# Kernel tuning notes

Measured on AMD Instinct MI355X. Metric: run time of the kernel, lower is better.

Reference implementation:

```python
import jax, jax.numpy as jnp
import numpy as np

B, I, M, A, HC, HR = 64, 10, 64, 16384, 256, 2
O = 8  # output_size = num_data_bits
EPS = 1e-8


def setup_inputs() -> dict:
    key = jax.random.key(0)
    ks = jax.random.split(key, 16)
    inputs = jax.random.normal(ks[0], (B, I), jnp.float32)
    # init_state: memory ~ N(0.5, 0.2)
    memory = 0.5 + 0.2 * jax.random.normal(ks[1], (B, M, A), jnp.float32)
    rw = jax.random.uniform(ks[2], (B, HR, A), jnp.float32)
    read_w = rw / rw.sum(-1, keepdims=True)           # normalized attention weights
    ww = jax.random.uniform(ks[3], (B, A), jnp.float32)
    write_w = ww / ww.sum(-1, keepdims=True)
    h = 0.1 * jax.random.normal(ks[4], (B, HC), jnp.float32)
    c = 0.1 * jax.random.normal(ks[5], (B, HC), jnp.float32)
    read_vecs = 0.1 * jax.random.normal(ks[6], (B, HR, M), jnp.float32)
    lstm_in = I + HR * M  # controller sees input ++ flattened read vectors
    sc = lambda n: 1.0 / np.sqrt(n)
    W_ih = sc(lstm_in) * jax.random.normal(ks[7], (4 * HC, lstm_in), jnp.float32)
    W_hh = sc(HC) * jax.random.normal(ks[8], (4 * HC, HC), jnp.float32)
    b_lstm = jnp.zeros((4 * HC,), jnp.float32)
    P = HR * (M + 6) + (3 * M + 6)  # 338
    W_int = sc(HC) * jax.random.normal(ks[9], (P, HC), jnp.float32)
    b_int = jnp.zeros((P,), jnp.float32)
    W_out = sc(HC) * jax.random.normal(ks[10], (O, HC), jnp.float32)
    b_out = jnp.zeros((O,), jnp.float32)
    return dict(inputs=inputs, memory=memory, read_w=read_w, write_w=write_w,
                h=h, c=c, read_vecs=read_vecs, W_ih=W_ih, W_hh=W_hh,
                b_lstm=b_lstm, W_int=W_int, b_int=b_int, W_out=W_out, b_out=b_out)


def _address(k, beta, g, s, gamma, w_prev, mem):
    """NTM addressing: content sim -> interpolate -> circular shift -> sharpen.
    k:[B,M] beta,g,gamma:[B,1] s:[B,3] w_prev:[B,A] mem:[B,M,A] -> [B,A]."""
    beta = jax.nn.softplus(beta)
    g = jax.nn.sigmoid(g)
    s = jax.nn.softmax(s, axis=-1)
    gamma = 1.0 + jax.nn.softplus(gamma)
    kn = k / (jnp.linalg.norm(k, axis=-1, keepdims=True) + EPS)
    mn = mem / (jnp.linalg.norm(mem, axis=1, keepdims=True) + EPS)
    sim = jnp.einsum('bm,bma->ba', kn, mn)          # cosine similarity
    wc = jax.nn.softmax(beta * sim, axis=-1)         # content weights
    wg = g * wc + (1.0 - g) * w_prev                 # interpolation gate
    ws = (s[:, 0:1] * jnp.roll(wg, -1, axis=-1)      # circular conv, shifts {-1,0,1}
          + s[:, 1:2] * wg
          + s[:, 2:3] * jnp.roll(wg, 1, axis=-1))
    wp = (ws + EPS) ** gamma                         # sharpening
    return wp / (wp.sum(-1, keepdims=True) + EPS)


def reference(inputs, memory, read_w, write_w, h, c, read_vecs,
              W_ih, W_hh, b_lstm, W_int, b_int, W_out, b_out):
    # --- LSTM controller: concat(input, read vectors) -> hidden ---
    x = jnp.concatenate([inputs, read_vecs.reshape(B, HR * M)], axis=-1)
    gates = x @ W_ih.T + h @ W_hh.T + b_lstm
    ig, fg, gg, og = jnp.split(gates, 4, axis=-1)
    c_new = jax.nn.sigmoid(fg) * c + jax.nn.sigmoid(ig) * jnp.tanh(gg)
    h_new = jax.nn.sigmoid(og) * jnp.tanh(c_new)
    # --- Interface parameter head ---
    p = h_new @ W_int.T + b_int
    off = 0
    read_params = []
    for _ in range(HR):
        blk = p[:, off:off + M + 6]; off += M + 6
        read_params.append((blk[:, :M], blk[:, M:M + 1], blk[:, M + 1:M + 2],
                            blk[:, M + 2:M + 5], blk[:, M + 5:M + 6]))
    wb = p[:, off:]
    kw, bw, gw, sw, gmw = wb[:, :M], wb[:, M:M + 1], wb[:, M + 1:M + 2], wb[:, M + 2:M + 5], wb[:, M + 5:M + 6]
    erase = jax.nn.sigmoid(wb[:, M + 6:2 * M + 6])   # [B,M]
    add = wb[:, 2 * M + 6:]                          # [B,M]
    # --- Write: address, erase/add rank-1 memory update ---
    w_wr = _address(kw, bw, gw, sw, gmw, write_w, memory)         # [B,A]
    mem_new = memory * (1.0 - erase[:, :, None] * w_wr[:, None, :]) \
              + add[:, :, None] * w_wr[:, None, :]
    # --- Read heads on updated memory ---
    rws, rvs = [], []
    for r in range(HR):
        w = _address(*read_params[r], read_w[:, r], mem_new)
        rws.append(w)
        rvs.append(jnp.einsum('bma,ba->bm', mem_new, w))
    logits = h_new @ W_out.T + b_out
    return (logits, mem_new, jnp.stack(rvs, 1), jnp.stack(rws, 1), w_wr, h_new, c_new)
```

## Files before the change

kernel.cpp:

```cpp
#include <hip/hip_runtime.h>
#include <math.h>

#define BB 64
#define ID 10
#define MD 64
#define AD 16384
#define HCD 256
#define HRD 2
#define OD 8
#define PD 338
#define EPSF 1e-8f

static constexpr size_t OFF_LOGITS = 0;
static constexpr size_t OFF_MEM = (size_t)BB * OD;
static constexpr size_t OFF_RVS = OFF_MEM + (size_t)BB * MD * AD;
static constexpr size_t OFF_RWS = OFF_RVS + (size_t)BB * HRD * MD;
static constexpr size_t OFF_WWR = OFF_RWS + (size_t)BB * HRD * AD;
static constexpr size_t OFF_H   = OFF_WWR + (size_t)BB * AD;
static constexpr size_t OFF_C   = OFF_H + (size_t)BB * HCD;

static constexpr size_t PAR = 0;
static constexpr size_t PAR_STR = 384;
static constexpr size_t EW   = PAR + (size_t)BB * PAR_STR;
static constexpr size_t ER   = EW + (size_t)BB * AD;
static constexpr size_t SUMS = ER + (size_t)2 * BB * AD;

__device__ __forceinline__ float sigmoidf_(float x) { return 1.f / (1.f + expf(-x)); }
__device__ __forceinline__ float softplusf_(float x) { return x > 20.f ? x : log1pf(expf(x)); }

__global__ __launch_bounds__(256) void k_small(
    const float* __restrict__ inputs, const float* __restrict__ read_vecs,
    const float* __restrict__ h, const float* __restrict__ c,
    const float* __restrict__ W_ih, const float* __restrict__ W_hh,
    const float* __restrict__ b_lstm, const float* __restrict__ W_int,
    const float* __restrict__ b_int, const float* __restrict__ W_out,
    const float* __restrict__ b_out, float* __restrict__ out,
    float* __restrict__ ws)
{
  const int b = blockIdx.x;
  const int t = threadIdx.x;
  __shared__ float sx[144];
  __shared__ float sh[HCD];
  __shared__ float sg[4 * HCD];
  __shared__ float shn[HCD];
  __shared__ float sp[PD];

  if (t < ID) sx[t] = inputs[(size_t)b * ID + t];
  else if (t < ID + HRD * MD) sx[t] = read_vecs[(size_t)b * HRD * MD + (t - ID)];
  if (t < HCD) sh[t] = h[(size_t)b * HCD + t];
  if (t < HRD * MD) out[OFF_RVS + (size_t)b * HRD * MD + t] = 0.f;
  if (t >= 128 && t < 136) ws[SUMS + (size_t)b * 8 + (t - 128)] = 0.f;
  __syncthreads();

  const int LIN = ID + HRD * MD;
  #pragma unroll
  for (int q = 0; q < 4; ++q) {
    int j = t + q * 256;
    const float* wr = W_ih + (size_t)j * LIN;
    float acc = b_lstm[j];
    for (int k = 0; k < LIN; ++k) acc += sx[k] * wr[k];
    const float* wh = W_hh + (size_t)j * HCD;
    for (int k = 0; k < HCD; ++k) acc += sh[k] * wh[k];
    sg[j] = acc;
  }
  __syncthreads();

  {
    float ig = sg[t], fg = sg[t + 256], gg = sg[t + 512], og = sg[t + 768];
    float cv = c[(size_t)b * HCD + t];
    float cn = sigmoidf_(fg) * cv + sigmoidf_(ig) * tanhf(gg);
    float hn = sigmoidf_(og) * tanhf(cn);
    shn[t] = hn;
    out[OFF_C + (size_t)b * HCD + t] = cn;
    out[OFF_H + (size_t)b * HCD + t] = hn;
  }
  __syncthreads();

  for (int j = t; j < PD; j += 256) {
    const float* wr = W_int + (size_t)j * HCD;
    float acc = b_int[j];
    for (int k = 0; k < HCD; ++k) acc += shn[k] * wr[k];
    sp[j] = acc;
  }
  if (t < OD) {
    const float* wr = W_out + (size_t)t * HCD;
    float acc = b_out[t];
    for (int k = 0; k < HCD; ++k) acc += shn[k] * wr[k];
    out[OFF_LOGITS + (size_t)b * OD + t] = acc;
  }
  __syncthreads();

  float* par = ws + PAR + (size_t)b * PAR_STR;
  const int wv = t >> 6, lane = t & 63;
  if (wv < 3) {
    const int base = (wv == 0) ? 140 : (wv - 1) * 70;
    const int slot = (wv == 0) ? 0 : (192 + (wv - 1) * 64);
    float kv = sp[base + lane];
    float ss = kv * kv;
    #pragma unroll
    for (int o = 32; o > 0; o >>= 1) ss += __shfl_xor(ss, o);
    par[slot + lane] = kv / (sqrtf(ss) + EPSF);
    if (lane == 0) {
      const int sb = (wv == 0) ? 320 : (326 + (wv - 1) * 6);
      float beta = softplusf_(sp[base + 64]);
      float g = sigmoidf_(sp[base + 65]);
      float s0 = sp[base + 66], s1 = sp[base + 67], s2 = sp[base + 68];
      float mx = fmaxf(s0, fmaxf(s1, s2));
      float e0 = expf(s0 - mx), e1 = expf(s1 - mx), e2 = expf(s2 - mx);
      float inv = 1.f / (e0 + e1 + e2);
      float gamma = 1.f + softplusf_(sp[base + 69]);
      par[sb + 0] = beta; par[sb + 1] = g;
      par[sb + 2] = e0 * inv; par[sb + 3] = e1 * inv; par[sb + 4] = e2 * inv;
      par[sb + 5] = gamma;
    }
  } else if (wv == 3) {
    par[64 + lane] = sigmoidf_(sp[210 + lane]);
    par[128 + lane] = sp[274 + lane];
  }
}

__global__ __launch_bounds__(256) void k_wsim(const float* __restrict__ mem,
                                              float* __restrict__ ws)
{
  const int b = blockIdx.y;
  const int tid = threadIdx.x;
  const size_t a0 = (size_t)blockIdx.x * 1024 + (size_t)tid * 4;
  const float* par = ws + PAR + (size_t)b * PAR_STR;
  __shared__ float kn[MD];
  if (tid < MD) kn[tid] = par[tid];
  __syncthreads();

  const float* mb = mem + (size_t)b * MD * AD + a0;
  float4 ssq = make_float4(0.f, 0.f, 0.f, 0.f);
  float4 dt  = make_float4(0.f, 0.f, 0.f, 0.f);
  for (int m = 0; m < MD; ++m) {
    float4 v = *(const float4*)(mb + (size_t)m * AD);
    float kv = kn[m];
    ssq.x += v.x * v.x; ssq.y += v.y * v.y; ssq.z += v.z * v.z; ssq.w += v.w * v.w;
    dt.x += kv * v.x;  dt.y += kv * v.y;  dt.z += kv * v.z;  dt.w += kv * v.w;
  }
  const float beta = par[320];
  float4 e;
  e.x = expf(beta * (dt.x / (sqrtf(ssq.x) + EPSF) - 1.f));
  e.y = expf(beta * (dt.y / (sqrtf(ssq.y) + EPSF) - 1.f));
  e.z = expf(beta * (dt.z / (sqrtf(ssq.z) + EPSF) - 1.f));
  e.w = expf(beta * (dt.w / (sqrtf(ssq.w) + EPSF) - 1.f));
  *(float4*)(ws + EW + (size_t)b * AD + a0) = e;

  float s = e.x + e.y + e.z + e.w;
  #pragma unroll
  for (int o = 32; o > 0; o >>= 1) s += __shfl_xor(s, o);
  __shared__ float red[4];
  if ((tid & 63) == 0) red[tid >> 6] = s;
  __syncthreads();
  if (tid == 0) atomicAdd(ws + SUMS + (size_t)b * 8 + 0, red[0] + red[1] + red[2] + red[3]);
}

__global__ __launch_bounds__(256) void k_wsharp(const float* __restrict__ write_w,
                                                float* __restrict__ out,
                                                float* __restrict__ ws)
{
  const int b = blockIdx.y;
  const int tid = threadIdx.x;
  const int a0 = blockIdx.x * 1024 + tid * 4;
  const float* par = ws + PAR + (size_t)b * PAR_STR;
  const float g = par[321], s0 = par[322], s1 = par[323], s2 = par[324], gamma = par[325];
  const float inv_se = 1.f / ws[SUMS + (size_t)b * 8 + 0];
  const float* e = ws + EW + (size_t)b * AD;
  const float* wprev = write_w + (size_t)b * AD;

  float wg[6];
  #pragma unroll
  for (int i = 0; i < 6; ++i) {
    int a = (a0 - 1 + i) & (AD - 1);
    wg[i] = g * e[a] * inv_se + (1.f - g) * wprev[a];
  }
  float4 wp;
  wp.x = powf(s0 * wg[2] + s1 * wg[1] + s2 * wg[0] + EPSF, gamma);
  wp.y = powf(s0 * wg[3] + s1 * wg[2] + s2 * wg[1] + EPSF, gamma);
  wp.z = powf(s0 * wg[4] + s1 * wg[3] + s2 * wg[2] + EPSF, gamma);
  wp.w = powf(s0 * wg[5] + s1 * wg[4] + s2 * wg[3] + EPSF, gamma);
  *(float4*)(out + OFF_WWR + (size_t)b * AD + a0) = wp;

  float s = wp.x + wp.y + wp.z + wp.w;
  #pragma unroll
  for (int o = 32; o > 0; o >>= 1) s += __shfl_xor(s, o);
  __shared__ float red[4];
  if ((tid & 63) == 0) red[tid >> 6] = s;
  __syncthreads();
  if (tid == 0) atomicAdd(ws + SUMS + (size_t)b * 8 + 1, red[0] + red[1] + red[2] + red[3]);
}

__global__ __launch_bounds__(256) void k_update(const float* __restrict__ mem,
                                                float* __restrict__ out,
                                                float* __restrict__ ws)
{
  const int b = blockIdx.y;
  const int tid = threadIdx.x;
  const size_t a0 = (size_t)blockIdx.x * 1024 + (size_t)tid * 4;
  const float* par = ws + PAR + (size_t)b * PAR_STR;
  __shared__ float se[MD], sa[MD], sk0[MD], sk1[MD];
  if (tid < MD) {
    se[tid] = par[64 + tid]; sa[tid] = par[128 + tid];
    sk0[tid] = par[192 + tid]; sk1[tid] = par[256 + tid];
  }
  __syncthreads();

  const float invw = 1.f / (ws[SUMS + (size_t)b * 8 + 1] + EPSF);
  float* wwr = out + OFF_WWR + (size_t)b * AD + a0;
  float4 w = *(float4*)wwr;
  w.x *= invw; w.y *= invw; w.z *= invw; w.w *= invw;
  *(float4*)wwr = w;

  const float* mb = mem + (size_t)b * MD * AD + a0;
  float* nb = out + OFF_MEM + (size_t)b * MD * AD + a0;
  float4 ssq = make_float4(0.f, 0.f, 0.f, 0.f);
  float4 d0 = make_float4(0.f, 0.f, 0.f, 0.f);
  float4 d1 = make_float4(0.f, 0.f, 0.f, 0.f);
  for (int m = 0; m < MD; ++m) {
    float4 v = *(const float4*)(mb + (size_t)m * AD);
    float er = se[m], ad = sa[m], k0 = sk0[m], k1 = sk1[m];
    float4 nv;
    nv.x = v.x * (1.f - er * w.x) + ad * w.x;
    nv.y = v.y * (1.f - er * w.y) + ad * w.y;
    nv.z = v.z * (1.f - er * w.z) + ad * w.z;
    nv.w = v.w * (1.f - er * w.w) + ad * w.w;
    *(float4*)(nb + (size_t)m * AD) = nv;
    ssq.x += nv.x * nv.x; ssq.y += nv.y * nv.y; ssq.z += nv.z * nv.z; ssq.w += nv.w * nv.w;
    d0.x += k0 * nv.x; d0.y += k0 * nv.y; d0.z += k0 * nv.z; d0.w += k0 * nv.w;
    d1.x += k1 * nv.x; d1.y += k1 * nv.y; d1.z += k1 * nv.z; d1.w += k1 * nv.w;
  }
  const float b0 = par[326], b1 = par[332];
  float4 e0, e1;
  e0.x = expf(b0 * (d0.x / (sqrtf(ssq.x) + EPSF) - 1.f));
  e0.y = expf(b0 * (d0.y / (sqrtf(ssq.y) + EPSF) - 1.f));
  e0.z = expf(b0 * (d0.z / (sqrtf(ssq.z) + EPSF) - 1.f));
  e0.w = expf(b0 * (d0.w / (sqrtf(ssq.w) + EPSF) - 1.f));
  e1.x = expf(b1 * (d1.x / (sqrtf(ssq.x) + EPSF) - 1.f));
  e1.y = expf(b1 * (d1.y / (sqrtf(ssq.y) + EPSF) - 1.f));
  e1.z = expf(b1 * (d1.z / (sqrtf(ssq.z) + EPSF) - 1.f));
  e1.w = expf(b1 * (d1.w / (sqrtf(ssq.w) + EPSF) - 1.f));
  *(float4*)(ws + ER + ((size_t)0 * BB + b) * AD + a0) = e0;
  *(float4*)(ws + ER + ((size_t)1 * BB + b) * AD + a0) = e1;

  float p0 = e0.x + e0.y + e0.z + e0.w;
  float p1 = e1.x + e1.y + e1.z + e1.w;
  #pragma unroll
  for (int o = 32; o > 0; o >>= 1) { p0 += __shfl_xor(p0, o); p1 += __shfl_xor(p1, o); }
  __shared__ float red[8];
  const int lane = tid & 63, wv = tid >> 6;
  if (lane == 0) { red[wv] = p0; red[4 + wv] = p1; }
  __syncthreads();
  if (tid == 0) atomicAdd(ws + SUMS + (size_t)b * 8 + 2, red[0] + red[1] + red[2] + red[3]);
  if (tid == 1) atomicAdd(ws + SUMS + (size_t)b * 8 + 3, red[4] + red[5] + red[6] + red[7]);
}

__global__ __launch_bounds__(256) void k_rsharp(const float* __restrict__ read_w,
                                                float* __restrict__ out,
                                                float* __restrict__ ws)
{
  const int b = blockIdx.y;
  const int hH = blockIdx.z;
  const int tid = threadIdx.x;
  const int a0 = blockIdx.x * 1024 + tid * 4;
  const float* par = ws + PAR + (size_t)b * PAR_STR;
  const int sb = 326 + hH * 6;
  const float g = par[sb + 1], s0 = par[sb + 2], s1 = par[sb + 3], s2 = par[sb + 4], gamma = par[sb + 5];
  const float inv_se = 1.f / ws[SUMS + (size_t)b * 8 + 2 + hH];
  const float* e = ws + ER + ((size_t)hH * BB + b) * AD;
  const float* wprev = read_w + ((size_t)b * HRD + hH) * AD;

  float wg[6];
  #pragma unroll
  for (int i = 0; i < 6; ++i) {
    int a = (a0 - 1 + i) & (AD - 1);
    wg[i] = g * e[a] * inv_se + (1.f - g) * wprev[a];
  }
  float4 wp;
  wp.x = powf(s0 * wg[2] + s1 * wg[1] + s2 * wg[0] + EPSF, gamma);
  wp.y = powf(s0 * wg[3] + s1 * wg[2] + s2 * wg[1] + EPSF, gamma);
  wp.z = powf(s0 * wg[4] + s1 * wg[3] + s2 * wg[2] + EPSF, gamma);
  wp.w = powf(s0 * wg[5] + s1 * wg[4] + s2 * wg[3] + EPSF, gamma);
  *(float4*)(out + OFF_RWS + ((size_t)b * HRD + hH) * AD + a0) = wp;

  float s = wp.x + wp.y + wp.z + wp.w;
  #pragma unroll
  for (int o = 32; o > 0; o >>= 1) s += __shfl_xor(s, o);
  __shared__ float red[4];
  if ((tid & 63) == 0) red[tid >> 6] = s;
  __syncthreads();
  if (tid == 0) atomicAdd(ws + SUMS + (size_t)b * 8 + 4 + hH, red[0] + red[1] + red[2] + red[3]);
}

__global__ __launch_bounds__(256) void k_readvec(float* __restrict__ out,
                                                 const float* __restrict__ ws)
{
  const int b = blockIdx.y;
  const int tid = threadIdx.x;
  const size_t a0 = (size_t)blockIdx.x * 1024 + (size_t)tid * 4;
  const float inv0 = 1.f / (ws[SUMS + (size_t)b * 8 + 4] + EPSF);
  const float inv1 = 1.f / (ws[SUMS + (size_t)b * 8 + 5] + EPSF);

  float* r0 = out + OFF_RWS + ((size_t)b * HRD + 0) * AD + a0;
  float* r1 = out + OFF_RWS + ((size_t)b * HRD + 1) * AD + a0;
  float4 w0 = *(float4*)r0;
  w0.x *= inv0; w0.y *= inv0; w0.z *= inv0; w0.w *= inv0;
  *(float4*)r0 = w0;
  float4 w1 = *(float4*)r1;
  w1.x *= inv1; w1.y *= inv1; w1.z *= inv1; w1.w *= inv1;
  *(float4*)r1 = w1;

  const float* mn = out + OFF_MEM + (size_t)b * MD * AD + a0;
  __shared__ float part[4][MD][2];
  const int lane = tid & 63, wv = tid >> 6;
  for (int m = 0; m < MD; ++m) {
    float4 v = *(const float4*)(mn + (size_t)m * AD);
    float p0 = v.x * w0.x + v.y * w0.y + v.z * w0.z + v.w * w0.w;
    float p1 = v.x * w1.x + v.y * w1.y + v.z * w1.z + v.w * w1.w;
    #pragma unroll
    for (int o = 32; o > 0; o >>= 1) { p0 += __shfl_xor(p0, o); p1 += __shfl_xor(p1, o); }
    if (lane == 0) { part[wv][m][0] = p0; part[wv][m][1] = p1; }
  }
  __syncthreads();
  if (tid < 128) {
    int hH = tid >> 6, m = tid & 63;
    float s = part[0][m][hH] + part[1][m][hH] + part[2][m][hH] + part[3][m][hH];
    atomicAdd(out + OFF_RVS + ((size_t)b * HRD + hH) * MD + m, s);
  }
}

extern "C" void kernel_launch(void* const* d_in, const int* in_sizes, int n_in,
                              void* d_out, int out_size, void* d_ws, size_t ws_size,
                              hipStream_t stream) {
  const float* inputs    = (const float*)d_in[0];
  const float* memory    = (const float*)d_in[1];
  const float* read_w    = (const float*)d_in[2];
  const float* write_w   = (const float*)d_in[3];
  const float* h         = (const float*)d_in[4];
  const float* c         = (const float*)d_in[5];
  const float* read_vecs = (const float*)d_in[6];
  const float* W_ih      = (const float*)d_in[7];
  const float* W_hh      = (const float*)d_in[8];
  const float* b_lstm    = (const float*)d_in[9];
  const float* W_int     = (const float*)d_in[10];
  const float* b_int     = (const float*)d_in[11];
  const float* W_out     = (const float*)d_in[12];
  const float* b_out     = (const float*)d_in[13];
  float* out = (float*)d_out;
  float* ws  = (float*)d_ws;

  hipLaunchKernelGGL(k_small, dim3(BB), dim3(256), 0, stream,
                     inputs, read_vecs, h, c, W_ih, W_hh, b_lstm, W_int, b_int,
                     W_out, b_out, out, ws);
  hipLaunchKernelGGL(k_wsim, dim3(AD / 1024, BB), dim3(256), 0, stream, memory, ws);
  hipLaunchKernelGGL(k_wsharp, dim3(AD / 1024, BB), dim3(256), 0, stream, write_w, out, ws);
  hipLaunchKernelGGL(k_update, dim3(AD / 1024, BB), dim3(256), 0, stream, memory, out, ws);
  hipLaunchKernelGGL(k_rsharp, dim3(AD / 1024, BB, HRD), dim3(256), 0, stream, read_w, out, ws);
  hipLaunchKernelGGL(k_readvec, dim3(AD / 1024, BB), dim3(256), 0, stream, out, ws);
}
```

Measured before the change: 735.3 us.

## Warp-cooperative LSTM matvecs and wider per-thread tiles for memory-streaming kernels

```diff
diff --git a/kernel.cpp b/kernel.cpp
--- a/kernel.cpp
+++ b/kernel.cpp
@@ -9,6 +9,7 @@
 #define HRD 2
 #define OD 8
 #define PD 338
+#define LIN 138
 #define EPSF 1e-8f
 
 static constexpr size_t OFF_LOGITS = 0;
@@ -39,29 +40,31 @@
 {
   const int b = blockIdx.x;
   const int t = threadIdx.x;
-  __shared__ float sx[144];
+  const int lane = t & 63, wv = t >> 6;
+  __shared__ float sx[LIN];
   __shared__ float sh[HCD];
   __shared__ float sg[4 * HCD];
   __shared__ float shn[HCD];
   __shared__ float sp[PD];
 
   if (t < ID) sx[t] = inputs[(size_t)b * ID + t];
-  else if (t < ID + HRD * MD) sx[t] = read_vecs[(size_t)b * HRD * MD + (t - ID)];
+  else if (t < LIN) sx[t] = read_vecs[(size_t)b * HRD * MD + (t - ID)];
   if (t < HCD) sh[t] = h[(size_t)b * HCD + t];
   if (t < HRD * MD) out[OFF_RVS + (size_t)b * HRD * MD + t] = 0.f;
   if (t >= 128 && t < 136) ws[SUMS + (size_t)b * 8 + (t - 128)] = 0.f;
   __syncthreads();
 
-  const int LIN = ID + HRD * MD;
-  #pragma unroll
-  for (int q = 0; q < 4; ++q) {
-    int j = t + q * 256;
+  for (int jj = 0; jj < 256; ++jj) {
+    const int j = wv * 256 + jj;
+    float acc = 0.f;
     const float* wr = W_ih + (size_t)j * LIN;
-    float acc = b_lstm[j];
-    for (int k = 0; k < LIN; ++k) acc += sx[k] * wr[k];
+    for (int k = lane; k < LIN; k += 64) acc += sx[k] * wr[k];
     const float* wh = W_hh + (size_t)j * HCD;
-    for (int k = 0; k < HCD; ++k) acc += sh[k] * wh[k];
-    sg[j] = acc;
+    #pragma unroll
+    for (int kk = 0; kk < 4; ++kk) acc += sh[lane + kk * 64] * wh[lane + kk * 64];
+    #pragma unroll
+    for (int o = 32; o > 0; o >>= 1) acc += __shfl_xor(acc, o);
+    if (lane == 0) sg[j] = acc + b_lstm[j];
   }
   __syncthreads();
 
@@ -76,22 +79,27 @@
   }
   __syncthreads();
 
-  for (int j = t; j < PD; j += 256) {
+  for (int j = wv; j < PD; j += 4) {
+    float acc = 0.f;
     const float* wr = W_int + (size_t)j * HCD;
-    float acc = b_int[j];
-    for (int k = 0; k < HCD; ++k) acc += shn[k] * wr[k];
-    sp[j] = acc;
-  }
-  if (t < OD) {
-    const float* wr = W_out + (size_t)t * HCD;
-    float acc = b_out[t];
-    for (int k = 0; k < HCD; ++k) acc += shn[k] * wr[k];
-    out[OFF_LOGITS + (size_t)b * OD + t] = acc;
+    #pragma unroll
+    for (int kk = 0; kk < 4; ++kk) acc += shn[lane + kk * 64] * wr[lane + kk * 64];
+    #pragma unroll
+    for (int o = 32; o > 0; o >>= 1) acc += __shfl_xor(acc, o);
+    if (lane == 0) sp[j] = acc + b_int[j];
+  }
+  for (int j = wv; j < OD; j += 4) {
+    float acc = 0.f;
+    const float* wr = W_out + (size_t)j * HCD;
+    #pragma unroll
+    for (int kk = 0; kk < 4; ++kk) acc += shn[lane + kk * 64] * wr[lane + kk * 64];
+    #pragma unroll
+    for (int o = 32; o > 0; o >>= 1) acc += __shfl_xor(acc, o);
+    if (lane == 0) out[OFF_LOGITS + (size_t)b * OD + j] = acc + b_out[j];
   }
   __syncthreads();
 
   float* par = ws + PAR + (size_t)b * PAR_STR;
-  const int wv = t >> 6, lane = t & 63;
   if (wv < 3) {
     const int base = (wv == 0) ? 140 : (wv - 1) * 70;
     const int slot = (wv == 0) ? 0 : (192 + (wv - 1) * 64);
@@ -113,47 +121,62 @@
       par[sb + 2] = e0 * inv; par[sb + 3] = e1 * inv; par[sb + 4] = e2 * inv;
       par[sb + 5] = gamma;
     }
-  } else if (wv == 3) {
+  } else {
     par[64 + lane] = sigmoidf_(sp[210 + lane]);
     par[128 + lane] = sp[274 + lane];
   }
 }
 
-__global__ __launch_bounds__(256) void k_wsim(const float* __restrict__ mem,
+
+__global__ __launch_bounds__(512) void k_wsim(const float* __restrict__ mem,
                                               float* __restrict__ ws)
 {
-  const int b = blockIdx.y;
-  const int tid = threadIdx.x;
-  const size_t a0 = (size_t)blockIdx.x * 1024 + (size_t)tid * 4;
+  const int b = blockIdx.y, tid = threadIdx.x, q = blockIdx.x;
   const float* par = ws + PAR + (size_t)b * PAR_STR;
   __shared__ float kn[MD];
   if (tid < MD) kn[tid] = par[tid];
   __syncthreads();
 
-  const float* mb = mem + (size_t)b * MD * AD + a0;
-  float4 ssq = make_float4(0.f, 0.f, 0.f, 0.f);
-  float4 dt  = make_float4(0.f, 0.f, 0.f, 0.f);
+  const size_t c0 = (size_t)q * 4096 + (size_t)tid * 4;
+  const size_t c1 = c0 + 2048;
+  const float* mb = mem + (size_t)b * MD * AD;
+
+  float4 sA = {0,0,0,0}, sB = {0,0,0,0}, dA = {0,0,0,0}, dB = {0,0,0,0};
+  #pragma unroll 4
   for (int m = 0; m < MD; ++m) {
-    float4 v = *(const float4*)(mb + (size_t)m * AD);
+    float4 vA = *(const float4*)(mb + (size_t)m * AD + c0);
+    float4 vB = *(const float4*)(mb + (size_t)m * AD + c1);
     float kv = kn[m];
-    ssq.x += v.x * v.x; ssq.y += v.y * v.y; ssq.z += v.z * v.z; ssq.w += v.w * v.w;
-    dt.x += kv * v.x;  dt.y += kv * v.y;  dt.z += kv * v.z;  dt.w += kv * v.w;
+    sA.x += vA.x * vA.x; sA.y += vA.y * vA.y; sA.z += vA.z * vA.z; sA.w += vA.w * vA.w;
+    sB.x += vB.x * vB.x; sB.y += vB.y * vB.y; sB.z += vB.z * vB.z; sB.w += vB.w * vB.w;
+    dA.x += kv * vA.x;  dA.y += kv * vA.y;  dA.z += kv * vA.z;  dA.w += kv * vA.w;
+    dB.x += kv * vB.x;  dB.y += kv * vB.y;  dB.z += kv * vB.z;  dB.w += kv * vB.w;
   }
   const float beta = par[320];
-  float4 e;
-  e.x = expf(beta * (dt.x / (sqrtf(ssq.x) + EPSF) - 1.f));
-  e.y = expf(beta * (dt.y / (sqrtf(ssq.y) + EPSF) - 1.f));
-  e.z = expf(beta * (dt.z / (sqrtf(ssq.z) + EPSF) - 1.f));
-  e.w = expf(beta * (dt.w / (sqrtf(ssq.w) + EPSF) - 1.f));
-  *(float4*)(ws + EW + (size_t)b * AD + a0) = e;
-
-  float s = e.x + e.y + e.z + e.w;
+  float4 eA, eB;
+  eA.x = expf(beta * (dA.x / (sqrtf(sA.x) + EPSF) - 1.f));
+  eA.y = expf(beta * (dA.y / (sqrtf(sA.y) + EPSF) - 1.f));
+  eA.z = expf(beta * (dA.z / (sqrtf(sA.z) + EPSF) - 1.f));
+  eA.w = expf(beta * (dA.w / (sqrtf(sA.w) + EPSF) - 1.f));
+  eB.x = expf(beta * (dB.x / (sqrtf(sB.x) + EPSF) - 1.f));
+  eB.y = expf(beta * (dB.y / (sqrtf(sB.y) + EPSF) - 1.f));
+  eB.z = expf(beta * (dB.z / (sqrtf(sB.z) + EPSF) - 1.f));
+  eB.w = expf(beta * (dB.w / (sqrtf(sB.w) + EPSF) - 1.f));
+  *(float4*)(ws + EW + (size_t)b * AD + c0) = eA;
+  *(float4*)(ws + EW + (size_t)b * AD + c1) = eB;
+
+  float s = eA.x + eA.y + eA.z + eA.w + eB.x + eB.y + eB.z + eB.w;
   #pragma unroll
   for (int o = 32; o > 0; o >>= 1) s += __shfl_xor(s, o);
-  __shared__ float red[4];
+  __shared__ float red[8];
   if ((tid & 63) == 0) red[tid >> 6] = s;
   __syncthreads();
-  if (tid == 0) atomicAdd(ws + SUMS + (size_t)b * 8 + 0, red[0] + red[1] + red[2] + red[3]);
+  if (tid == 0) {
+    float tot = 0.f;
+    #pragma unroll
+    for (int i = 0; i < 8; ++i) tot += red[i];
+    atomicAdd(ws + SUMS + (size_t)b * 8 + 0, tot);
+  }
 }
 
 __global__ __launch_bounds__(256) void k_wsharp(const float* __restrict__ write_w,
@@ -169,12 +192,15 @@
   const float* e = ws + EW + (size_t)b * AD;
   const float* wprev = write_w + (size_t)b * AD;
 
+  float4 ec = *(const float4*)(e + a0);
+  float4 wc = *(const float4*)(wprev + a0);
+  const int am1 = (a0 - 1) & (AD - 1), ap4 = (a0 + 4) & (AD - 1);
+  float ev[6] = {e[am1], ec.x, ec.y, ec.z, ec.w, e[ap4]};
+  float wvv[6] = {wprev[am1], wc.x, wc.y, wc.z, wc.w, wprev[ap4]};
   float wg[6];
   #pragma unroll
-  for (int i = 0; i < 6; ++i) {
-    int a = (a0 - 1 + i) & (AD - 1);
-    wg[i] = g * e[a] * inv_se + (1.f - g) * wprev[a];
-  }
+  for (int i = 0; i < 6; ++i) wg[i] = g * ev[i] * inv_se + (1.f - g) * wvv[i];
+
   float4 wp;
   wp.x = powf(s0 * wg[2] + s1 * wg[1] + s2 * wg[0] + EPSF, gamma);
   wp.y = powf(s0 * wg[3] + s1 * wg[2] + s2 * wg[1] + EPSF, gamma);
@@ -191,13 +217,11 @@
   if (tid == 0) atomicAdd(ws + SUMS + (size_t)b * 8 + 1, red[0] + red[1] + red[2] + red[3]);
 }
 
-__global__ __launch_bounds__(256) void k_update(const float* __restrict__ mem,
+__global__ __launch_bounds__(512) void k_update(const float* __restrict__ mem,
                                                 float* __restrict__ out,
                                                 float* __restrict__ ws)
 {
-  const int b = blockIdx.y;
-  const int tid = threadIdx.x;
-  const size_t a0 = (size_t)blockIdx.x * 1024 + (size_t)tid * 4;
+  const int b = blockIdx.y, tid = threadIdx.x, q = blockIdx.x;
   const float* par = ws + PAR + (size_t)b * PAR_STR;
   __shared__ float se[MD], sa[MD], sk0[MD], sk1[MD];
   if (tid < MD) {
@@ -206,53 +230,82 @@
   }
   __syncthreads();
 
+  const size_t c0 = (size_t)q * 4096 + (size_t)tid * 4;
+  const size_t c1 = c0 + 2048;
   const float invw = 1.f / (ws[SUMS + (size_t)b * 8 + 1] + EPSF);
-  float* wwr = out + OFF_WWR + (size_t)b * AD + a0;
-  float4 w = *(float4*)wwr;
-  w.x *= invw; w.y *= invw; w.z *= invw; w.w *= invw;
-  *(float4*)wwr = w;
-
-  const float* mb = mem + (size_t)b * MD * AD + a0;
-  float* nb = out + OFF_MEM + (size_t)b * MD * AD + a0;
-  float4 ssq = make_float4(0.f, 0.f, 0.f, 0.f);
-  float4 d0 = make_float4(0.f, 0.f, 0.f, 0.f);
-  float4 d1 = make_float4(0.f, 0.f, 0.f, 0.f);
+  float* wwr = out + OFF_WWR + (size_t)b * AD;
+  float4 wA = *(float4*)(wwr + c0);
+  float4 wB = *(float4*)(wwr + c1);
+  wA.x *= invw; wA.y *= invw; wA.z *= invw; wA.w *= invw;
+  wB.x *= invw; wB.y *= invw; wB.z *= invw; wB.w *= invw;
+  *(float4*)(wwr + c0) = wA;
+  *(float4*)(wwr + c1) = wB;
+
+  const float* mb = mem + (size_t)b * MD * AD;
+  float* nb = out + OFF_MEM + (size_t)b * MD * AD;
+  float4 sA = {0,0,0,0}, sB = {0,0,0,0};
+  float4 d0A = {0,0,0,0}, d0B = {0,0,0,0}, d1A = {0,0,0,0}, d1B = {0,0,0,0};
+  #pragma unroll 4
   for (int m = 0; m < MD; ++m) {
-    float4 v = *(const float4*)(mb + (size_t)m * AD);
+    float4 vA = *(const float4*)(mb + (size_t)m * AD + c0);
+    float4 vB = *(const float4*)(mb + (size_t)m * AD + c1);
     float er = se[m], ad = sa[m], k0 = sk0[m], k1 = sk1[m];
-    float4 nv;
-    nv.x = v.x * (1.f - er * w.x) + ad * w.x;
-    nv.y = v.y * (1.f - er * w.y) + ad * w.y;
-    nv.z = v.z * (1.f - er * w.z) + ad * w.z;
-    nv.w = v.w * (1.f - er * w.w) + ad * w.w;
-    *(float4*)(nb + (size_t)m * AD) = nv;
-    ssq.x += nv.x * nv.x; ssq.y += nv.y * nv.y; ssq.z += nv.z * nv.z; ssq.w += nv.w * nv.w;
-    d0.x += k0 * nv.x; d0.y += k0 * nv.y; d0.z += k0 * nv.z; d0.w += k0 * nv.w;
-    d1.x += k1 * nv.x; d1.y += k1 * nv.y; d1.z += k1 * nv.z; d1.w += k1 * nv.w;
+    float4 nA, nB;
+    nA.x = vA.x * (1.f - er * wA.x) + ad * wA.x;
+    nA.y = vA.y * (1.f - er * wA.y) + ad * wA.y;
+    nA.z = vA.z * (1.f - er * wA.z) + ad * wA.z;
+    nA.w = vA.w * (1.f - er * wA.w) + ad * wA.w;
+    nB.x = vB.x * (1.f - er * wB.x) + ad * wB.x;
+    nB.y = vB.y * (1.f - er * wB.y) + ad * wB.y;
+    nB.z = vB.z * (1.f - er * wB.z) + ad * wB.z;
+    nB.w = vB.w * (1.f - er * wB.w) + ad * wB.w;
+    *(float4*)(nb + (size_t)m * AD + c0) = nA;
+    *(float4*)(nb + (size_t)m * AD + c1) = nB;
+    sA.x += nA.x * nA.x; sA.y += nA.y * nA.y; sA.z += nA.z * nA.z; sA.w += nA.w * nA.w;
+    sB.x += nB.x * nB.x; sB.y += nB.y * nB.y; sB.z += nB.z * nB.z; sB.w += nB.w * nB.w;
+    d0A.x += k0 * nA.x; d0A.y += k0 * nA.y; d0A.z += k0 * nA.z; d0A.w += k0 * nA.w;
+    d0B.x += k0 * nB.x; d0B.y += k0 * nB.y; d0B.z += k0 * nB.z; d0B.w += k0 * nB.w;
+    d1A.x += k1 * nA.x; d1A.y += k1 * nA.y; d1A.z += k1 * nA.z; d1A.w += k1 * nA.w;
+    d1B.x += k1 * nB.x; d1B.y += k1 * nB.y; d1B.z += k1 * nB.z; d1B.w += k1 * nB.w;
   }
   const float b0 = par[326], b1 = par[332];
-  float4 e0, e1;
-  e0.x = expf(b0 * (d0.x / (sqrtf(ssq.x) + EPSF) - 1.f));
-  e0.y = expf(b0 * (d0.y / (sqrtf(ssq.y) + EPSF) - 1.f));
-  e0.z = expf(b0 * (d0.z / (sqrtf(ssq.z) + EPSF) - 1.f));
-  e0.w = expf(b0 * (d0.w / (sqrtf(ssq.w) + EPSF) - 1.f));
-  e1.x = expf(b1 * (d1.x / (sqrtf(ssq.x) + EPSF) - 1.f));
-  e1.y = expf(b1 * (d1.y / (sqrtf(ssq.y) + EPSF) - 1.f));
-  e1.z = expf(b1 * (d1.z / (sqrtf(ssq.z) + EPSF) - 1.f));
-  e1.w = expf(b1 * (d1.w / (sqrtf(ssq.w) + EPSF) - 1.f));
-  *(float4*)(ws + ER + ((size_t)0 * BB + b) * AD + a0) = e0;
-  *(float4*)(ws + ER + ((size_t)1 * BB + b) * AD + a0) = e1;
-
-  float p0 = e0.x + e0.y + e0.z + e0.w;
-  float p1 = e1.x + e1.y + e1.z + e1.w;
+  float4 e0A, e0B, e1A, e1B;
+  e0A.x = expf(b0 * (d0A.x / (sqrtf(sA.x) + EPSF) - 1.f));
+  e0A.y = expf(b0 * (d0A.y / (sqrtf(sA.y) + EPSF) - 1.f));
+  e0A.z = expf(b0 * (d0A.z / (sqrtf(sA.z) + EPSF) - 1.f));
+  e0A.w = expf(b0 * (d0A.w / (sqrtf(sA.w) + EPSF) - 1.f));
+  e0B.x = expf(b0 * (d0B.x / (sqrtf(sB.x) + EPSF) - 1.f));
+  e0B.y = expf(b0 * (d0B.y / (sqrtf(sB.y) + EPSF) - 1.f));
+  e0B.z = expf(b0 * (d0B.z / (sqrtf(sB.z) + EPSF) - 1.f));
+  e0B.w = expf(b0 * (d0B.w / (sqrtf(sB.w) + EPSF) - 1.f));
+  e1A.x = expf(b1 * (d1A.x / (sqrtf(sA.x) + EPSF) - 1.f));
+  e1A.y = expf(b1 * (d1A.y / (sqrtf(sA.y) + EPSF) - 1.f));
+  e1A.z = expf(b1 * (d1A.z / (sqrtf(sA.z) + EPSF) - 1.f));
+  e1A.w = expf(b1 * (d1A.w / (sqrtf(sA.w) + EPSF) - 1.f));
+  e1B.x = expf(b1 * (d1B.x / (sqrtf(sB.x) + EPSF) - 1.f));
+  e1B.y = expf(b1 * (d1B.y / (sqrtf(sB.y) + EPSF) - 1.f));
+  e1B.z = expf(b1 * (d1B.z / (sqrtf(sB.z) + EPSF) - 1.f));
+  e1B.w = expf(b1 * (d1B.w / (sqrtf(sB.w) + EPSF) - 1.f));
+  float* er0 = ws + ER + ((size_t)0 * BB + b) * AD;
+  float* er1 = ws + ER + ((size_t)1 * BB + b) * AD;
+  *(float4*)(er0 + c0) = e0A; *(float4*)(er0 + c1) = e0B;
+  *(float4*)(er1 + c0) = e1A; *(float4*)(er1 + c1) = e1B;
+
+  float p0 = e0A.x + e0A.y + e0A.z + e0A.w + e0B.x + e0B.y + e0B.z + e0B.w;
+  float p1 = e1A.x + e1A.y + e1A.z + e1A.w + e1B.x + e1B.y + e1B.z + e1B.w;
   #pragma unroll
   for (int o = 32; o > 0; o >>= 1) { p0 += __shfl_xor(p0, o); p1 += __shfl_xor(p1, o); }
-  __shared__ float red[8];
+  __shared__ float red[16];
   const int lane = tid & 63, wv = tid >> 6;
-  if (lane == 0) { red[wv] = p0; red[4 + wv] = p1; }
-  __syncthreads();
-  if (tid == 0) atomicAdd(ws + SUMS + (size_t)b * 8 + 2, red[0] + red[1] + red[2] + red[3]);
-  if (tid == 1) atomicAdd(ws + SUMS + (size_t)b * 8 + 3, red[4] + red[5] + red[6] + red[7]);
+  if (lane == 0) { red[wv] = p0; red[8 + wv] = p1; }
+  __syncthreads();
+  if (tid == 0) {
+    float t0 = 0.f, t1 = 0.f;
+    #pragma unroll
+    for (int i = 0; i < 8; ++i) { t0 += red[i]; t1 += red[8 + i]; }
+    atomicAdd(ws + SUMS + (size_t)b * 8 + 2, t0);
+    atomicAdd(ws + SUMS + (size_t)b * 8 + 3, t1);
+  }
 }
 
 __global__ __launch_bounds__(256) void k_rsharp(const float* __restrict__ read_w,
@@ -270,12 +323,15 @@
   const float* e = ws + ER + ((size_t)hH * BB + b) * AD;
   const float* wprev = read_w + ((size_t)b * HRD + hH) * AD;
 
+  float4 ec = *(const float4*)(e + a0);
+  float4 wc = *(const float4*)(wprev + a0);
+  const int am1 = (a0 - 1) & (AD - 1), ap4 = (a0 + 4) & (AD - 1);
+  float ev[6] = {e[am1], ec.x, ec.y, ec.z, ec.w, e[ap4]};
+  float wvv[6] = {wprev[am1], wc.x, wc.y, wc.z, wc.w, wprev[ap4]};
   float wg[6];
   #pragma unroll
-  for (int i = 0; i < 6; ++i) {
-    int a = (a0 - 1 + i) & (AD - 1);
-    wg[i] = g * e[a] * inv_se + (1.f - g) * wprev[a];
-  }
+  for (int i = 0; i < 6; ++i) wg[i] = g * ev[i] * inv_se + (1.f - g) * wvv[i];
+
   float4 wp;
   wp.x = powf(s0 * wg[2] + s1 * wg[1] + s2 * wg[0] + EPSF, gamma);
   wp.y = powf(s0 * wg[3] + s1 * wg[2] + s2 * wg[1] + EPSF, gamma);
@@ -292,39 +348,46 @@
   if (tid == 0) atomicAdd(ws + SUMS + (size_t)b * 8 + 4 + hH, red[0] + red[1] + red[2] + red[3]);
 }
 
-__global__ __launch_bounds__(256) void k_readvec(float* __restrict__ out,
-                                                 const float* __restrict__ ws)
-{
-  const int b = blockIdx.y;
-  const int tid = threadIdx.x;
-  const size_t a0 = (size_t)blockIdx.x * 1024 + (size_t)tid * 4;
+__global__ __launch_bounds__(512) void k_rv(float* __restrict__ out,
+                                            const float* __restrict__ ws)
+{
+  const int b = blockIdx.y, tid = threadIdx.x, q = blockIdx.x;
+  const size_t c0 = (size_t)q * 4096 + (size_t)tid * 4;
+  const size_t c1 = c0 + 2048;
   const float inv0 = 1.f / (ws[SUMS + (size_t)b * 8 + 4] + EPSF);
   const float inv1 = 1.f / (ws[SUMS + (size_t)b * 8 + 5] + EPSF);
 
-  float* r0 = out + OFF_RWS + ((size_t)b * HRD + 0) * AD + a0;
-  float* r1 = out + OFF_RWS + ((size_t)b * HRD + 1) * AD + a0;
-  float4 w0 = *(float4*)r0;
-  w0.x *= inv0; w0.y *= inv0; w0.z *= inv0; w0.w *= inv0;
-  *(float4*)r0 = w0;
-  float4 w1 = *(float4*)r1;
-  w1.x *= inv1; w1.y *= inv1; w1.z *= inv1; w1.w *= inv1;
-  *(float4*)r1 = w1;
-
-  const float* mn = out + OFF_MEM + (size_t)b * MD * AD + a0;
-  __shared__ float part[4][MD][2];
+  float* r0 = out + OFF_RWS + ((size_t)b * HRD + 0) * AD;
+  float* r1 = out + OFF_RWS + ((size_t)b * HRD + 1) * AD;
+  float4 w0A = *(float4*)(r0 + c0), w0B = *(float4*)(r0 + c1);
+  float4 w1A = *(float4*)(r1 + c0), w1B = *(float4*)(r1 + c1);
+  w0A.x *= inv0; w0A.y *= inv0; w0A.z *= inv0; w0A.w *= inv0;
+  w0B.x *= inv0; w0B.y *= inv0; w0B.z *= inv0; w0B.w *= inv0;
+  w1A.x *= inv1; w1A.y *= inv1; w1A.z *= inv1; w1A.w *= inv1;
+  w1B.x *= inv1; w1B.y *= inv1; w1B.z *= inv1; w1B.w *= inv1;
+  *(float4*)(r0 + c0) = w0A; *(float4*)(r0 + c1) = w0B;
+  *(float4*)(r1 + c0) = w1A; *(float4*)(r1 + c1) = w1B;
+
+  const float* mn = out + OFF_MEM + (size_t)b * MD * AD;
+  __shared__ float part[8][MD][2];
   const int lane = tid & 63, wv = tid >> 6;
   for (int m = 0; m < MD; ++m) {
-    float4 v = *(const float4*)(mn + (size_t)m * AD);
-    float p0 = v.x * w0.x + v.y * w0.y + v.z * w0.z + v.w * w0.w;
-    float p1 = v.x * w1.x + v.y * w1.y + v.z * w1.z + v.w * w1.w;
+    float4 vA = *(const float4*)(mn + (size_t)m * AD + c0);
+    float4 vB = *(const float4*)(mn + (size_t)m * AD + c1);
+    float p0 = vA.x * w0A.x + vA.y * w0A.y + vA.z * w0A.z + vA.w * w0A.w
+             + vB.x * w0B.x + vB.y * w0B.y + vB.z * w0B.z + vB.w * w0B.w;
+    float p1 = vA.x * w1A.x + vA.y * w1A.y + vA.z * w1A.z + vA.w * w1A.w
+             + vB.x * w1B.x + vB.y * w1B.y + vB.z * w1B.z + vB.w * w1B.w;
     #pragma unroll
     for (int o = 32; o > 0; o >>= 1) { p0 += __shfl_xor(p0, o); p1 += __shfl_xor(p1, o); }
     if (lane == 0) { part[wv][m][0] = p0; part[wv][m][1] = p1; }
   }
   __syncthreads();
   if (tid < 128) {
-    int hH = tid >> 6, m = tid & 63;
-    float s = part[0][m][hH] + part[1][m][hH] + part[2][m][hH] + part[3][m][hH];
+    const int hH = tid >> 6, m = tid & 63;
+    float s = 0.f;
+    #pragma unroll
+    for (int i = 0; i < 8; ++i) s += part[i][m][hH];
     atomicAdd(out + OFF_RVS + ((size_t)b * HRD + hH) * MD + m, s);
   }
 }
@@ -352,9 +415,9 @@
   hipLaunchKernelGGL(k_small, dim3(BB), dim3(256), 0, stream,
                      inputs, read_vecs, h, c, W_ih, W_hh, b_lstm, W_int, b_int,
                      W_out, b_out, out, ws);
-  hipLaunchKernelGGL(k_wsim, dim3(AD / 1024, BB), dim3(256), 0, stream, memory, ws);
+  hipLaunchKernelGGL(k_wsim, dim3(4, BB), dim3(512), 0, stream, memory, ws);
   hipLaunchKernelGGL(k_wsharp, dim3(AD / 1024, BB), dim3(256), 0, stream, write_w, out, ws);
-  hipLaunchKernelGGL(k_update, dim3(AD / 1024, BB), dim3(256), 0, stream, memory, out, ws);
+  hipLaunchKernelGGL(k_update, dim3(4, BB), dim3(512), 0, stream, memory, out, ws);
   hipLaunchKernelGGL(k_rsharp, dim3(AD / 1024, BB, HRD), dim3(256), 0, stream, read_w, out, ws);
-  hipLaunchKernelGGL(k_readvec, dim3(AD / 1024, BB), dim3(256), 0, stream, out, ws);
-}
+  hipLaunchKernelGGL(k_rv, dim3(4, BB), dim3(512), 0, stream, out, ws);
+}
```

After: 1.086 ms. 47.7% more time.
